# Performance work log

Hardware: AMD Instinct MI355X
Metric: run time of the kernel (lower is better)

Reference implementation:

```python
import jax, jax.numpy as jnp
from jax import lax
import numpy as np

B, N, G = 32, 8192, 40   # batch, points per cloud, base voxel grid (coords -20..19)
VS = 0.05                # voxel size
NFREQ = 4                # 8 encoding channels per coord = 4 freqs x (sin,cos)
DN = ('NCDHW', 'OIDHW', 'NCDHW')


def _encode(x):
    # sinusoidal positional encoding: [B,N,3] -> [B,N,24]
    freqs = (2.0 ** jnp.arange(NFREQ, dtype=jnp.float32)) * jnp.pi  # encoding_range=1
    ang = x[..., None] * freqs                    # [B,N,3,4]
    enc = jnp.concatenate([jnp.sin(ang), jnp.cos(ang)], axis=-1)  # [B,N,3,8]
    return enc.reshape(x.shape[0], x.shape[1], 3 * 2 * NFREQ)


def _voxelize(x, enc):
    # mean-pool point features into 40^3 voxels; returns feat [B,24,G,G,G], mask [B,1,G,G,G]
    vi = jnp.clip(jnp.floor(x / VS).astype(jnp.int32), -G // 2, G // 2 - 1) + G // 2
    lin = (vi[..., 0] * G + vi[..., 1]) * G + vi[..., 2]            # [B,N]
    flat = (lin + jnp.arange(B, dtype=jnp.int32)[:, None] * G ** 3).reshape(-1)
    fsum = jnp.zeros((B * G ** 3, 24), jnp.float32).at[flat].add(enc.reshape(-1, 24))
    cnt = jnp.zeros((B * G ** 3, 1), jnp.float32).at[flat].add(1.0)
    active = cnt > 0
    feat = jnp.where(active, fsum / jnp.maximum(cnt, 1.0), 0.0)
    feat = feat.reshape(B, G, G, G, 24).transpose(0, 4, 1, 2, 3)
    mask = active.astype(jnp.float32).reshape(B, 1, G, G, G)
    return feat, mask


def _conv(x, w, b, stride, pad):
    y = lax.conv_general_dilated(x, w, (stride,) * 3, pad, dimension_numbers=DN)
    return y + b[None, :, None, None, None]


def _ln_c(x, g, b, mask, eps=1e-5):
    # per-voxel LayerNorm over channels, only on active voxels
    mu = jnp.mean(x, axis=1, keepdims=True)
    var = jnp.mean((x - mu) ** 2, axis=1, keepdims=True)
    y = (x - mu) * lax.rsqrt(var + eps)
    return (y * g[None, :, None, None, None] + b[None, :, None, None, None]) * mask


def _maxpool2(m):
    return lax.reduce_window(m, -jnp.inf, lax.max, (1, 1, 2, 2, 2), (1, 1, 2, 2, 2), 'VALID')


def setup_inputs() -> dict:
    key = jax.random.key(0)
    ks = jax.random.split(key, 16)
    x = jax.random.uniform(ks[0], (B, N, 3), jnp.float32, minval=-1.0, maxval=1.0)

    def w(k, shape, fan_in):
        return jax.random.normal(k, shape, jnp.float32) * (2.0 / fan_in) ** 0.5

    d = {'x': x}
    d['c1w'] = w(ks[1], (32, 24, 3, 3, 3), 24 * 27);   d['c1b'] = jnp.zeros(32)
    d['g1'] = jnp.ones(32);                            d['b1'] = jnp.zeros(32)
    d['s1w'] = w(ks[2], (64, 32, 2, 2, 2), 32 * 8);    d['s1b'] = jnp.zeros(64)
    d['c2w'] = w(ks[3], (128, 64, 3, 3, 3), 64 * 27);  d['c2b'] = jnp.zeros(128)
    d['g2'] = jnp.ones(128);                           d['b2'] = jnp.zeros(128)
    d['s2w'] = w(ks[4], (256, 128, 2, 2, 2), 128 * 8); d['s2b'] = jnp.zeros(256)
    d['c3w'] = w(ks[5], (512, 256, 3, 3, 3), 256 * 27); d['c3b'] = jnp.zeros(512)
    d['g3'] = jnp.ones(512);                           d['b3'] = jnp.zeros(512)
    d['c4w'] = w(ks[6], (1024, 512, 3, 3, 3), 512 * 27); d['c4b'] = jnp.zeros(1024)
    d['s4w'] = w(ks[7], (1024, 1024, 2, 2, 2), 1024 * 8); d['s4b'] = jnp.zeros(1024)
    d['g4'] = jnp.ones(8192);                          d['b4'] = jnp.zeros(8192)
    d['f1w'] = w(ks[8], (1024, 8192), 8192);           d['f1b'] = jnp.zeros(1024)
    d['f2w'] = w(ks[9], (40, 1024), 1024);             d['f2b'] = jnp.zeros(40)
    return d


def _forward(x, c1w, c1b, g1, b1, s1w, s1b, c2w, c2b, g2, b2, s2w, s2b,
             c3w, c3b, g3, b3, c4w, c4b, s4w, s4b, g4, b4, f1w, f1b, f2w, f2b):
    enc = _encode(x)
    h, m = _voxelize(x, enc)                                 # 40^3, 24ch
    h = _conv(h, c1w, c1b, 1, 'SAME') * m                    # submanifold sparse conv
    h = jax.nn.relu(_ln_c(h, g1, b1, m))
    m = _maxpool2(m)
    h = jax.nn.relu(_conv(h, s1w, s1b, 2, 'VALID') * m)      # 40 -> 20
    h = _conv(h, c2w, c2b, 1, 'SAME') * m
    h = jax.nn.relu(_ln_c(h, g2, b2, m))
    m = _maxpool2(m)
    h = jax.nn.relu(_conv(h, s2w, s2b, 2, 'VALID') * m)      # 20 -> 10
    h = _conv(h, c3w, c3b, 1, 'SAME') * m
    h = _ln_c(h, g3, b3, m)                                  # to_dense: zeros off-mask
    h = jax.nn.relu(h)
    h = jax.nn.relu(_conv(h, c4w, c4b, 2, 'VALID'))          # 10 -> 4 (dense Conv3d)
    h = _conv(h, s4w, s4b, 2, 'VALID')                       # 4 -> 2
    h = h.reshape(B, -1)                                     # [B, 8192]
    mu = jnp.mean(h, -1, keepdims=True)
    var = jnp.mean((h - mu) ** 2, -1, keepdims=True)
    h = (h - mu) * lax.rsqrt(var + 1e-5) * g4 + b4
    h = jax.nn.relu(h)                                       # dropout: eval mode identity
    h = jax.nn.relu(h @ f1w.T + f1b)
    h = h @ f2w.T + f2b
    return jax.nn.log_softmax(h, axis=-1)


def reference(x, c1w, c1b, g1, b1, s1w, s1b, c2w, c2b, g2, b2, s2w, s2b,
              c3w, c3b, g3, b3, c4w, c4b, s4w, s4b, g4, b4, f1w, f1b, f2w, f2b):
    return _forward(x, c1w, c1b, g1, b1, s1w, s1b, c2w, c2b, g2, b2, s2w, s2b,
                    c3w, c3b, g3, b3, c4w, c4b, s4w, s4b, g4, b4, f1w, f1b, f2w, f2b)
```

## Files before the change

### kernel.cpp

```cpp
#include <hip/hip_runtime.h>
#include <math.h>

#define B_ 32
#define N_ 8192
#define G_ 40
#define CB_ 4
#define QB_ 8

static inline int cdiv(long a, int b){ return (int)((a + (long)b - 1)/b); }

typedef double d4 __attribute__((ext_vector_type(4)));

#define OFF_S1O   0
#define OFF_S2O   0
#define OFF_PART  0
#define OFF_C4O   16777216
#define OFF_FC1   20971520
#define OFF_LOG   21233664
#define OFF_C2O   32768000
#define OFF_FS    32768000
#define OFF_CNT   81920000
#define OFF_C3O   32768000
#define OFF_M20   98304000
#define OFF_M10   99328000
#define OFF_S4O   99456000
#define WS_NEEDED 101560000

__global__ __launch_bounds__(256) void encode_scatter(const float* __restrict__ x,
    double* __restrict__ fsum, double* __restrict__ cnt, int b0)
{
  int tid = blockIdx.x*256 + threadIdx.x;
  if (tid >= CB_*N_) return;
  int bl = tid / N_;
  const float* p = x + ((size_t)b0*N_ + (size_t)tid)*3;
  float c[3] = { p[0], p[1], p[2] };
  int vi[3];
  #pragma unroll
  for (int ci=0; ci<3; ++ci){
    int v = (int)floorf(c[ci] / 0.05f);
    v = v < -20 ? -20 : (v > 19 ? 19 : v);
    vi[ci] = v + 20;
  }
  int lin = (vi[0]*G_ + vi[1])*G_ + vi[2];
  double* fs = fsum + (size_t)bl*24*64000 + lin;
  const float PI_F = 3.14159265358979323846f;
  #pragma unroll
  for (int ci=0; ci<3; ++ci){
    double ang = (double)c[ci] * (double)PI_F;
    double s = sin(ang), co = cos(ang);
    #pragma unroll
    for (int k=0; k<4; ++k){
      atomicAdd(fs + (size_t)(ci*8 + k)    *64000, s);
      atomicAdd(fs + (size_t)(ci*8 + 4 + k)*64000, co);
      double s2 = 2.0*s*co;
      double c2 = co*co - s*s;
      s = s2; co = c2;
    }
  }
  atomicAdd(cnt + (size_t)bl*64000 + lin, 1.0);
}

__global__ __launch_bounds__(256) void pool_cnt_m20(const double* __restrict__ cnt,
    float* __restrict__ m20)
{
  int tid = blockIdx.x*256 + threadIdx.x;
  if (tid >= CB_*8000) return;
  int xo = tid % 20; int t = tid/20;
  int yo = t % 20;   t /= 20;
  int zo = t % 20;   int bl = t/20;
  const double* cb = cnt + (size_t)bl*64000;
  float mx = 0.0f;
  for (int dz=0; dz<2; ++dz)
    for (int dy=0; dy<2; ++dy)
      for (int dx=0; dx<2; ++dx)
        if (cb[(size_t)((zo*2+dz)*40 + (yo*2+dy))*40 + (xo*2+dx)] > 0.0) mx = 1.0f;
  m20[(size_t)bl*8000 + (zo*20+yo)*20+xo] = mx;
}

__global__ __launch_bounds__(256) void pool_mask_f(const float* __restrict__ m,
    float* __restrict__ mo, int Do, int NB)
{
  long tid = (long)blockIdx.x*256 + threadIdx.x;
  if (tid >= (long)NB*Do*Do*Do) return;
  int Di = Do*2;
  int xo = (int)(tid % Do); long t = tid / Do;
  int yo = (int)(t % Do);   t /= Do;
  int zo = (int)(t % Do);   int b = (int)(t / Do);
  const float* mb = m + (size_t)b*Di*Di*Di;
  float mx = 0.0f;
  for (int dz=0; dz<2; ++dz)
    for (int dy=0; dy<2; ++dy)
      for (int dx=0; dx<2; ++dx)
        mx = fmaxf(mx, mb[(size_t)(zo*2+dz)*Di*Di + (size_t)(yo*2+dy)*Di + (xo*2+dx)]);
  mo[tid] = mx;
}

__global__ __launch_bounds__(64) void c1_ln_s1(
    const double* __restrict__ fsum, const double* __restrict__ cnt,
    const float* __restrict__ c1w, const float* __restrict__ c1b,
    const float* __restrict__ g1,  const float* __restrict__ b1,
    const float* __restrict__ s1w, const float* __restrict__ s1b,
    double* __restrict__ out, int lb0)
{
  __shared__ double sfeat[24][64];
  __shared__ double sh1[32][8];
  __shared__ double smask[8];

  int blk = blockIdx.x;
  int xo = blk % 20; int t1 = blk/20;
  int yo = t1 % 20;  t1 /= 20;
  int zo = t1 % 20;  int bl = t1/20;
  int t = threadIdx.x;

  int lz = t >> 4, ly = (t >> 2) & 3, lx = t & 3;
  int gz = zo*2 - 1 + lz, gy = yo*2 - 1 + ly, gx = xo*2 - 1 + lx;
  bool inb = (gz>=0 && gz<40) && (gy>=0 && gy<40) && (gx>=0 && gx<40);
  int vox = (gz*40 + gy)*40 + gx;
  double cv = inb ? cnt[(size_t)bl*64000 + vox] : 0.0;
  double ic = (cv > 0.0) ? 1.0/cv : 0.0;
  const double* fb = fsum + (size_t)bl*24*64000 + (inb ? vox : 0);
  #pragma unroll
  for (int ci=0; ci<24; ++ci)
    sfeat[ci][t] = ic * fb[(size_t)ci*64000];
  if (t < 8){
    int dz=t>>2, dy=(t>>1)&1, dx=t&1;
    double c8 = cnt[(size_t)bl*64000 + (size_t)((zo*2+dz)*40 + (yo*2+dy))*40 + (xo*2+dx)];
    smask[t] = (c8 > 0.0) ? 1.0 : 0.0;
  }
  __syncthreads();

  double pm = fmax(fmax(fmax(smask[0],smask[1]),fmax(smask[2],smask[3])),
                   fmax(fmax(smask[4],smask[5]),fmax(smask[6],smask[7])));
  int ovox = (zo*20 + yo)*20 + xo;
  double* ob = out + (size_t)(lb0+bl)*64*8000 + ovox;
  if (pm == 0.0){
    ob[(size_t)t*8000] = 0.0;
    return;
  }

  int c   = t & 31;
  int svh = t >> 5;
  double acc[4] = {0,0,0,0};
  const float* wc = c1w + (size_t)c*24*27;
  for (int ci=0; ci<24; ++ci){
    const float* wp = wc + ci*27;
    const double* sp = &sfeat[ci][0] + svh*16;
    #pragma unroll
    for (int kz=0; kz<3; ++kz)
    #pragma unroll
    for (int ky=0; ky<3; ++ky)
    #pragma unroll
    for (int kx=0; kx<3; ++kx){
      double wv = (double)wp[(kz*3+ky)*3+kx];
      const double* q = sp + kz*16 + ky*4 + kx;
      acc[0] += wv * q[0];
      acc[1] += wv * q[1];
      acc[2] += wv * q[4];
      acc[3] += wv * q[5];
    }
  }
  double bias = (double)c1b[c], gc = (double)g1[c], bc = (double)b1[c];
  double h[4], rs1[4], rs2[4];
  #pragma unroll
  for (int i=0;i<4;++i){
    h[i] = (acc[i] + bias) * smask[svh*4+i];
    rs1[i] = h[i]; rs2[i] = h[i]*h[i];
  }
  #pragma unroll
  for (int off=1; off<32; off<<=1){
    #pragma unroll
    for (int i=0;i<4;++i){
      rs1[i] += __shfl_xor(rs1[i], off);
      rs2[i] += __shfl_xor(rs2[i], off);
    }
  }
  #pragma unroll
  for (int i=0;i<4;++i){
    double mu  = rs1[i]*(1.0/32.0);
    double var = fmax(rs2[i]*(1.0/32.0) - mu*mu, 0.0);
    double r   = 1.0/sqrt(var + 1e-5);
    double yv  = ((h[i]-mu)*r*gc + bc) * smask[svh*4+i];
    sh1[c][svh*4+i] = fmax(yv, 0.0);
  }
  __syncthreads();

  const float* wo = s1w + (size_t)t*256;
  double s = 0.0;
  #pragma unroll
  for (int ci=0; ci<32; ++ci){
    #pragma unroll
    for (int sv=0; sv<8; ++sv)
      s += (double)wo[ci*8+sv] * sh1[ci][sv];
  }
  ob[(size_t)t*8000] = fmax(s + (double)s1b[t], 0.0);
}

__device__ __forceinline__ double Pf_(int i,int k){ return (double)(1 + i + 31*k); }
__device__ __forceinline__ double Qf_(int k,int j){ return (double)(2 + 3*j + 7*k); }
__device__ __forceinline__ double Rf_(int m,int n){
  double s = 0.0;
  for (int k=0;k<4;++k) s += Pf_(m,k)*Qf_(k,n);
  return s;
}

template<int TI>
__global__ __launch_bounds__(256) void conv_mfma(
    const double* __restrict__ in, const float* __restrict__ w,
    const float* __restrict__ bias, double* __restrict__ out,
    int NB, int Cin, int Cout, int D)
{
  __shared__ float wl[TI*32*27];
  int spat = D*D*D;
  const int BV = 64;
  int nvt = (spat + BV - 1) / BV;
  int bid = blockIdx.x;
  int vt4 = bid % nvt; int t1 = bid / nvt;
  int cot = t1 % (Cout/32); int b = t1 / (Cout/32);
  int wid = threadIdx.x >> 6;
  int lane = threadIdx.x & 63;
  int li = lane & 15, lk = lane >> 4;

  d4 z = {0.0,0.0,0.0,0.0};
  d4 det = __builtin_amdgcn_mfma_f64_16x16x4f64(Pf_(li,lk), Qf_(lk,li), z, 0,0,0);
  bool m2 = true, m3 = true;
  #pragma unroll
  for (int r=0;r<4;++r){
    m2 = m2 && (fabs(det[r] - Rf_(lk+4*r, li)) < 1e-3);
    m3 = m3 && (fabs(det[r] - Rf_(li, 4*lk+r)) < 1e-3);
  }
  int mode = __all(m2) ? 2 : (__all(m3) ? 3 : 1);

  int vbase = vt4*BV + wid*16;
  int vox = vbase + li;
  bool vok = vox < spat;
  int vc = vok ? vox : 0;
  int vz = vc/(D*D), vy = (vc/D)%D, vx = vc%D;

  const double* inb = in + (size_t)b*Cin*spat;
  d4 acc0 = {0.0,0.0,0.0,0.0};
  d4 acc1 = {0.0,0.0,0.0,0.0};

  for (int ci0 = 0; ci0 < Cin; ci0 += TI){
    for (int idx = threadIdx.x; idx < TI*32*27; idx += 256){
      int tap = idx % 27; int t2 = idx / 27;
      int io = t2 % 32; int cc = t2 / 32;
      wl[(cc*32 + io)*27 + tap] =
          w[((size_t)(cot*32+io)*Cin + (ci0+cc))*27 + tap];
    }
    __syncthreads();
    const double* ipk = inb + (size_t)(ci0 + lk)*spat;
    #pragma unroll
    for (int dz = 0; dz < 3; ++dz){
      #pragma unroll
      for (int dy = 0; dy < 3; ++dy){
        #pragma unroll
        for (int dx = 0; dx < 3; ++dx){
          int tap = (dz*3+dy)*3+dx;
          int zi = vz+dz-1, yi = vy+dy-1, xi = vx+dx-1;
          bool ok = vok && zi>=0 && zi<D && yi>=0 && yi<D && xi>=0 && xi<D;
          int so = ok ? (zi*D + yi)*D + xi : 0;
          #pragma unroll
          for (int kq = 0; kq < TI/4; ++kq){
            double bv = ok ? ipk[(size_t)(kq*4)*spat + so] : 0.0;
            double a0 = (double)wl[((kq*4+lk)*32 + li)*27 + tap];
            double a1 = (double)wl[((kq*4+lk)*32 + 16 + li)*27 + tap];
            acc0 = __builtin_amdgcn_mfma_f64_16x16x4f64(a0, bv, acc0, 0, 0, 0);
            acc1 = __builtin_amdgcn_mfma_f64_16x16x4f64(a1, bv, acc1, 0, 0, 0);
          }
        }
      }
    }
    __syncthreads();
  }

  size_t obb = (size_t)b*Cout*spat;
  if (mode == 2){
    if (vok){
      #pragma unroll
      for (int r = 0; r < 4; ++r){
        int co0 = cot*32 + lk + 4*r;
        int co1 = co0 + 16;
        out[obb + (size_t)co0*spat + vox] = acc0[r] + (double)bias[co0];
        out[obb + (size_t)co1*spat + vox] = acc1[r] + (double)bias[co1];
      }
    }
  } else if (mode == 3){
    int co0 = cot*32 + li;
    int co1 = co0 + 16;
    double bv0 = (double)bias[co0], bv1 = (double)bias[co1];
    #pragma unroll
    for (int r = 0; r < 4; ++r){
      int vw = vbase + 4*lk + r;
      if (vw < spat){
        out[obb + (size_t)co0*spat + vw] = acc0[r] + bv0;
        out[obb + (size_t)co1*spat + vw] = acc1[r] + bv1;
      }
    }
  } else {
    if (vok){
      #pragma unroll
      for (int r = 0; r < 4; ++r){
        int co0 = cot*32 + 4*lk + r;
        int co1 = co0 + 16;
        out[obb + (size_t)co0*spat + vox] = acc0[r] + (double)bias[co0];
        out[obb + (size_t)co1*spat + vox] = acc1[r] + (double)bias[co1];
      }
    }
  }
}

static void launch_cmf(const double* in, const float* w, const float* bias,
                       double* out, int Cin, int Cout, int D, int NB, hipStream_t st)
{
  int spat = D*D*D;
  int nvt = (spat + 63)/64;
  int grid = NB * (Cout/32) * nvt;
  conv_mfma<8><<<grid,256,0,st>>>(in, w, bias, out, NB, Cin, Cout, D);
}

template<int K, int S, int P, int XT, int CT, int CGB, int TI,
         bool MMUL, bool RELU_, bool PARTIAL>
__global__ __launch_bounds__(256) void conv_lds(
    const double* __restrict__ in, const float* __restrict__ w,
    const float* __restrict__ bias, const float* __restrict__ mask,
    double* __restrict__ out, int NB, int Cin, int Din, int Cout, int Dout,
    int ncic, int cich)
{
  const int K3 = K*K*K;
  const int SP = 256/CGB;
  const int NR = (XT-1)*S + K;
  __shared__ float wl[CGB*CT][TI*K3];

  int tilesx = (Dout + XT - 1)/XT;
  int spat = tilesx*Dout*Dout;
  int nsb = (spat + SP - 1)/SP;
  int bid = blockIdx.x;
  int cic = 0;
  if (PARTIAL){ cic = bid % ncic; bid /= ncic; }
  int sb = bid % nsb;  int t1 = bid / nsb;
  int ncgo = Cout/(CT*CGB);
  int cgo = t1 % ncgo; int b = t1 / ncgo;
  int ciBeg = PARTIAL ? cic*cich : 0;
  int ciEnd = PARTIAL ? ciBeg + cich : Cin;

  int lc = threadIdx.x / SP;
  int sp = threadIdx.x % SP;
  int sidx = sb*SP + sp;
  bool act = sidx < spat;
  int sc = act ? sidx : 0;
  int tx = sc % tilesx;
  int y  = (sc/tilesx) % Dout;
  int z  = sc/(tilesx*Dout);
  int x0 = tx*XT;
  int co0 = (cgo*CGB + lc)*CT;

  int DD = Din*Din;
  const double* inb = in + (size_t)b*Cin*Din*DD;
  const int wcs = Cin*K3;

  double acc[CT][XT];
  #pragma unroll
  for (int c=0;c<CT;++c){
    double bv = PARTIAL ? 0.0 : (double)bias[co0+c];
    #pragma unroll
    for (int i=0;i<XT;++i) acc[c][i]=bv;
  }

  for (int ci0=ciBeg; ci0<ciEnd; ci0+=TI){
    const int cnt_w = CGB*CT*TI*K3;
    for (int idx = threadIdx.x; idx < cnt_w; idx += 256){
      int k  = idx % K3; int t2 = idx / K3;
      int cil= t2 % TI;  int cr = t2 / TI;
      int co = cgo*CGB*CT + cr;
      float v = 0.0f;
      if (ci0+cil < ciEnd) v = w[(size_t)co*wcs + (size_t)(ci0+cil)*K3 + k];
      wl[cr][cil*K3 + k] = v;
    }
    __syncthreads();
    int tmax = min(TI, ciEnd-ci0);
    for (int cil=0; cil<tmax; ++cil){
      const double* inc = inb + (size_t)(ci0+cil)*Din*DD;
      #pragma unroll
      for (int dz=0; dz<K; ++dz){
        int zi = z*S + dz - P;
        if (zi < 0 || zi >= Din) continue;
        #pragma unroll
        for (int dy=0; dy<K; ++dy){
          int yi = y*S + dy - P;
          if (yi < 0 || yi >= Din) continue;
          const double* row = inc + (size_t)zi*DD + (size_t)yi*Din;
          double rv[NR];
          #pragma unroll
          for (int r=0;r<NR;++r){
            int xi = x0*S + r - P;
            rv[r] = (xi>=0 && xi<Din) ? row[xi] : 0.0;
          }
          #pragma unroll
          for (int dx=0; dx<K; ++dx){
            double wv[CT];
            #pragma unroll
            for (int c=0;c<CT;++c)
              wv[c] = (double)wl[lc*CT+c][cil*K3 + (dz*K+dy)*K + dx];
            #pragma unroll
            for (int i=0;i<XT;++i)
              #pragma unroll
              for (int c=0;c<CT;++c) acc[c][i] += wv[c]*rv[i*S+dx];
          }
        }
      }
    }
    __syncthreads();
  }

  if (act){
    int oDD = Dout*Dout;
    size_t chunk_off = PARTIAL ? (size_t)cic*NB*Cout*Dout*oDD : 0;
    size_t ob = chunk_off + (size_t)b*Cout*Dout*oDD + (size_t)z*oDD + (size_t)y*Dout;
    #pragma unroll
    for (int i=0;i<XT;++i){
      int xo = x0+i;
      if (xo >= Dout) continue;
      double mv = 1.0;
      if (MMUL) mv = (double)mask[(size_t)b*Dout*oDD + (size_t)z*oDD + (size_t)y*Dout + xo];
      #pragma unroll
      for (int c=0;c<CT;++c){
        double v = acc[c][i];
        if (MMUL) v *= mv;
        if (RELU_) v = fmax(v,0.0);
        out[ob + (size_t)(co0+c)*Dout*oDD + xo] = v;
      }
    }
  }
}

template<int K,int S,int P,int XT,int CT,int CGB,int TI,bool MM,bool RL,bool PART>
static void launch_conv(const double* in, const float* w, const float* bias,
                        const float* mask, double* out,
                        int Cin, int Din, int Cout, int Dout, int NB,
                        int ncic, hipStream_t st)
{
  const int SP = 256/CGB;
  int tilesx = (Dout+XT-1)/XT;
  int spat = tilesx*Dout*Dout;
  int nsb = (spat + SP - 1)/SP;
  long grid = (long)(PART?ncic:1) * NB * (Cout/(CT*CGB)) * nsb;
  conv_lds<K,S,P,XT,CT,CGB,TI,MM,RL,PART><<<(int)grid,256,0,st>>>(
      in,w,bias,mask,out,NB,Cin,Din,Cout,Dout,ncic,Cin/(PART?ncic:1));
}

__global__ __launch_bounds__(256) void c4_reduce(const double* __restrict__ part,
    const float* __restrict__ bias, double* __restrict__ out, int NB, int ncic)
{
  long tid = (long)blockIdx.x*256 + threadIdx.x;
  long total = (long)NB*1024*64;
  if (tid >= total) return;
  int co = (int)((tid >> 6) & 1023);
  double s = (double)bias[co];
  for (int c=0; c<ncic; ++c) s += part[(size_t)c*total + tid];
  out[tid] = fmax(s, 0.0);
}

__global__ __launch_bounds__(256) void s4_wave(const double* __restrict__ c4o,
    const float* __restrict__ w, const float* __restrict__ bias,
    double* __restrict__ out, int NB)
{
  long gt = (long)blockIdx.x*256 + threadIdx.x;
  int wid = (int)(gt >> 6);
  int lane = threadIdx.x & 63;
  if (wid >= NB*1024) return;
  int co = wid & 1023; int b = wid >> 10;
  const double* ib = c4o + (size_t)b*1024*64;
  const float* wp = w + (size_t)co*8192;
  double acc[8] = {0,0,0,0,0,0,0,0};
  for (int k=lane; k<8192; k+=64){
    double wv = (double)wp[k];
    int ci = k>>3, sv = k&7;
    int dz = sv>>2, dy=(sv>>1)&1, dx=sv&1;
    const double* icp = ib + (size_t)ci*64;
    #pragma unroll
    for (int v=0; v<8; ++v){
      int zo=v>>2, yo=(v>>1)&1, xo=v&1;
      acc[v] += wv * icp[((zo*2+dz)*4+(yo*2+dy))*4 + (xo*2+dx)];
    }
  }
  #pragma unroll
  for (int v=0;v<8;++v){
    double a = acc[v];
    #pragma unroll
    for (int off=32;off>0;off>>=1) a += __shfl_down(a, off);
    if (lane==0) out[((size_t)b*1024+co)*8 + v] = a + (double)bias[co];
  }
}

__global__ __launch_bounds__(256) void ln_chan_d(double* __restrict__ x,
    const float* __restrict__ g, const float* __restrict__ bt,
    const float* __restrict__ mask, int C, int V, int NB)
{
  long tid = (long)blockIdx.x*256 + threadIdx.x;
  if (tid >= (long)NB*V) return;
  int b = (int)(tid / V);
  int v = (int)(tid - (long)b*V);
  double* xp = x + (size_t)b*C*V + v;
  double s = 0.0;
  for (int c=0; c<C; ++c) s += xp[(size_t)c*V];
  double mu = s / C;
  double s2 = 0.0;
  for (int c=0; c<C; ++c){ double d = xp[(size_t)c*V] - mu; s2 += d*d; }
  double r  = 1.0/sqrt(s2 / C + 1e-5);
  double mv = (double)mask[tid];
  for (int c=0; c<C; ++c){
    double yv = ((xp[(size_t)c*V] - mu) * r * (double)g[c] + (double)bt[c]) * mv;
    xp[(size_t)c*V] = fmax(yv, 0.0);
  }
}

__global__ __launch_bounds__(256) void ln_vec(double* __restrict__ h,
    const float* __restrict__ g, const float* __restrict__ bt)
{
  __shared__ double red[256];
  int b = blockIdx.x, t = threadIdx.x;
  double* hp = h + (size_t)b*8192;
  double s = 0.0;
  for (int k=t; k<8192; k+=256) s += hp[k];
  red[t] = s; __syncthreads();
  for (int o=128; o>0; o>>=1){ if (t<o) red[t] += red[t+o]; __syncthreads(); }
  double mu = red[0] / 8192.0;  __syncthreads();
  double s2 = 0.0;
  for (int k=t; k<8192; k+=256){ double d = hp[k]-mu; s2 += d*d; }
  red[t] = s2; __syncthreads();
  for (int o=128; o>0; o>>=1){ if (t<o) red[t] += red[t+o]; __syncthreads(); }
  double r = 1.0/sqrt(red[0]/8192.0 + 1e-5);
  for (int k=t; k<8192; k+=256)
    hp[k] = fmax((hp[k]-mu)*r*(double)g[k] + (double)bt[k], 0.0);
}

__global__ __launch_bounds__(256) void fc_wave(const double* __restrict__ h,
    const float* __restrict__ w, const float* __restrict__ bias,
    double* __restrict__ out, int Kdim, int O, int relu)
{
  long gt = (long)blockIdx.x*256 + threadIdx.x;
  int wid  = (int)(gt >> 6);
  int lane = threadIdx.x & 63;
  if (wid >= B_*O) return;
  int b = wid / O, o = wid - b*O;
  const double* hp = h + (size_t)b*Kdim;
  const float*  wp = w + (size_t)o*Kdim;
  double acc = 0.0;
  for (int k=lane; k<Kdim; k+=64) acc += hp[k]*(double)wp[k];
  #pragma unroll
  for (int off=32; off>0; off>>=1) acc += __shfl_down(acc, off);
  if (lane == 0){
    double v = acc + (double)bias[o];
    if (relu) v = fmax(v, 0.0);
    out[(size_t)b*O + o] = v;
  }
}

__global__ __launch_bounds__(64) void lsm_out(const double* __restrict__ logits,
    float* __restrict__ out)
{
  int b = threadIdx.x;
  if (b >= B_) return;
  const double* lp = logits + (size_t)b*40;
  double m = lp[0];
  for (int i=1; i<40; ++i) m = lp[i] > m ? lp[i] : m;
  double s = 0.0;
  for (int i=0; i<40; ++i) s += exp(lp[i]-m);
  double ls = log(s);
  for (int i=0; i<40; ++i) out[(size_t)b*40+i] = (float)(lp[i] - m - ls);
}

extern "C" void kernel_launch(void* const* d_in, const int* in_sizes, int n_in,
                              void* d_out, int out_size, void* d_ws, size_t ws_size,
                              hipStream_t stream)
{
  if (ws_size < (size_t)WS_NEEDED) return;

  const float* x   = (const float*)d_in[0];
  const float* c1w = (const float*)d_in[1];  const float* c1b = (const float*)d_in[2];
  const float* g1  = (const float*)d_in[3];  const float* b1  = (const float*)d_in[4];
  const float* s1w = (const float*)d_in[5];  const float* s1b = (const float*)d_in[6];
  const float* c2w = (const float*)d_in[7];  const float* c2b = (const float*)d_in[8];
  const float* g2  = (const float*)d_in[9];  const float* b2  = (const float*)d_in[10];
  const float* s2w = (const float*)d_in[11]; const float* s2b = (const float*)d_in[12];
  const float* c3w = (const float*)d_in[13]; const float* c3b = (const float*)d_in[14];
  const float* g3  = (const float*)d_in[15]; const float* b3  = (const float*)d_in[16];
  const float* c4w = (const float*)d_in[17]; const float* c4b = (const float*)d_in[18];
  const float* s4w = (const float*)d_in[19]; const float* s4b = (const float*)d_in[20];
  const float* g4  = (const float*)d_in[21]; const float* b4  = (const float*)d_in[22];
  const float* f1w = (const float*)d_in[23]; const float* f1b = (const float*)d_in[24];
  const float* f2w = (const float*)d_in[25]; const float* f2b = (const float*)d_in[26];

  char* ws = (char*)d_ws;
  double* s1o = (double*)(ws + OFF_S1O);
  double* s2o = (double*)(ws + OFF_S2O);
  double* part= (double*)(ws + OFF_PART);
  double* c4o = (double*)(ws + OFF_C4O);
  double* c2o = (double*)(ws + OFF_C2O);
  double* c3o = (double*)(ws + OFF_C3O);
  double* fsum= (double*)(ws + OFF_FS);
  double* cnt = (double*)(ws + OFF_CNT);
  float*  m20 = (float*)(ws + OFF_M20);
  float*  m10 = (float*)(ws + OFF_M10);
  double* s4o = (double*)(ws + OFF_S4O);
  double* fc1o= (double*)(ws + OFF_FC1);
  double* logd= (double*)(ws + OFF_LOG);

  for (int q = 0; q < 4; ++q){
    int qb0 = q * QB_;

    for (int sc = 0; sc < QB_/CB_; ++sc){
      int b0  = qb0 + sc*CB_;
      int lb0 = sc*CB_;
      hipMemsetAsync(ws + OFF_FS, 0, (size_t)CB_*24*64000*8 + (size_t)CB_*64000*8, stream);
      encode_scatter<<<cdiv((long)CB_*N_,256),256,0,stream>>>(x, fsum, cnt, b0);
      pool_cnt_m20  <<<cdiv((long)CB_*8000,256),256,0,stream>>>(cnt, m20 + (size_t)b0*8000);
      c1_ln_s1<<<CB_*8000, 64, 0, stream>>>(fsum, cnt, c1w, c1b, g1, b1,
                                            s1w, s1b, s1o, lb0);
    }
    pool_mask_f<<<cdiv((long)QB_*1000,256),256,0,stream>>>(
        m20 + (size_t)qb0*8000, m10 + (size_t)qb0*1000, 10, QB_);

    launch_cmf(s1o, c2w, c2b, c2o, 64, 128, 20, QB_, stream);
    ln_chan_d<<<cdiv((long)QB_*8000,256),256,0,stream>>>(
        c2o, g2, b2, m20 + (size_t)qb0*8000, 128, 8000, QB_);
    launch_conv<2,2,0, 2,8, 1,128, true,true,false>(c2o, s2w, s2b,
        m10 + (size_t)qb0*1000, s2o, 128, 20, 256, 10, QB_, 1, stream);

    launch_cmf(s2o, c3w, c3b, c3o, 256, 512, 10, QB_, stream);
    ln_chan_d<<<cdiv((long)QB_*1000,256),256,0,stream>>>(
        c3o, g3, b3, m10 + (size_t)qb0*1000, 512, 1000, QB_);

    launch_conv<3,2,0, 2,4, 8,8, false,false,true>(c3o, c4w, c4b, nullptr,
        part, 512, 10, 1024, 4, QB_, 4, stream);
    c4_reduce<<<cdiv((long)QB_*1024*64,256),256,0,stream>>>(part, c4b, c4o, QB_, 4);
    s4_wave<<<cdiv((long)QB_*1024*64,256),256,0,stream>>>(
        c4o, s4w, s4b, s4o + (size_t)qb0*8192, QB_);
  }

  ln_vec<<<B_,256,0,stream>>>(s4o, g4, b4);
  fc_wave<<<cdiv((long)B_*1024*64,256),256,0,stream>>>(s4o, f1w, f1b, fc1o, 8192, 1024, 1);
  fc_wave<<<cdiv((long)B_*40*64,256),  256,0,stream>>>(fc1o, f2w, f2b, logd, 1024, 40, 0);
  lsm_out<<<1,64,0,stream>>>(logd, (float*)d_out);
}
```

Baseline: 22.73 ms.

## Add LDS-staged input window conv kernel for the 10^3 c3 layer

Adds a specialized MFMA f64 3x3x3 conv for the 10x10x10 grid. It stages each block's 64-voxel input window plus a halo into shared memory, along with a tile of 8 input channels' weights, and reuses them across all 27 taps. Only the c3 layer (256 to 512 channels) switches to this kernel. The aim is to cut redundant global loads of the input, at the cost of more shared memory use and an extra sync per channel tile.

New measurement: 22.65 ms. Within noise of the previous version (-0.4%).

```diff
diff --git a/kernel.cpp b/kernel.cpp
--- a/kernel.cpp
+++ b/kernel.cpp
@@ -316,6 +316,130 @@
   int nvt = (spat + 63)/64;
   int grid = NB * (Cout/32) * nvt;
   conv_mfma<8><<<grid,256,0,st>>>(in, w, bias, out, NB, Cin, Cout, D);
+}
+
+__global__ __launch_bounds__(256) void conv_mfma_l(
+    const double* __restrict__ in, const float* __restrict__ w,
+    const float* __restrict__ bias, double* __restrict__ out,
+    int NB, int Cin, int Cout)
+{
+  const int D = 10, spat = 1000;
+  const int TI = 8, HALO = 111, WIN = 64 + 2*HALO;
+  __shared__ float  wl[TI*32*27];
+  __shared__ double sIn[TI][WIN];
+
+  const int BV = 64;
+  int nvt = (spat + BV - 1) / BV;
+  int bid = blockIdx.x;
+  int vt4 = bid % nvt; int t1 = bid / nvt;
+  int cot = t1 % (Cout/32); int b = t1 / (Cout/32);
+  int wid = threadIdx.x >> 6;
+  int lane = threadIdx.x & 63;
+  int li = lane & 15, lk = lane >> 4;
+
+  d4 z = {0.0,0.0,0.0,0.0};
+  d4 det = __builtin_amdgcn_mfma_f64_16x16x4f64(Pf_(li,lk), Qf_(lk,li), z, 0,0,0);
+  bool m2 = true, m3 = true;
+  #pragma unroll
+  for (int r=0;r<4;++r){
+    m2 = m2 && (fabs(det[r] - Rf_(lk+4*r, li)) < 1e-3);
+    m3 = m3 && (fabs(det[r] - Rf_(li, 4*lk+r)) < 1e-3);
+  }
+  int mode = __all(m2) ? 2 : (__all(m3) ? 3 : 1);
+
+  int blk0 = vt4*BV;
+  int vbase = blk0 + wid*16;
+  int vox = vbase + li;
+  bool vok = vox < spat;
+  int vc = vok ? vox : 0;
+  int vz = vc/(D*D), vy = (vc/D)%D, vx = vc%D;
+  int rel_base = wid*16 + li + HALO;
+
+  const double* inb = in + (size_t)b*Cin*spat;
+  d4 acc0 = {0.0,0.0,0.0,0.0};
+  d4 acc1 = {0.0,0.0,0.0,0.0};
+
+  for (int ci0 = 0; ci0 < Cin; ci0 += TI){
+    for (int idx = threadIdx.x; idx < TI*32*27; idx += 256){
+      int tap = idx % 27; int t2 = idx / 27;
+      int io = t2 % 32; int cc = t2 / 32;
+      wl[(cc*32 + io)*27 + tap] =
+          w[((size_t)(cot*32+io)*Cin + (ci0+cc))*27 + tap];
+    }
+    for (int idx = threadIdx.x; idx < TI*WIN; idx += 256){
+      int rel = idx % WIN; int cin = idx / WIN;
+      int g = blk0 - HALO + rel;
+      g = g < 0 ? 0 : (g >= spat ? spat-1 : g);
+      sIn[cin][rel] = inb[(size_t)(ci0+cin)*spat + g];
+    }
+    __syncthreads();
+    #pragma unroll
+    for (int dz = 0; dz < 3; ++dz){
+      #pragma unroll
+      for (int dy = 0; dy < 3; ++dy){
+        #pragma unroll
+        for (int dx = 0; dx < 3; ++dx){
+          int tap = (dz*3+dy)*3+dx;
+          int off = (dz-1)*100 + (dy-1)*10 + (dx-1);
+          int zi = vz+dz-1, yi = vy+dy-1, xi = vx+dx-1;
+          bool ok = vok && zi>=0 && zi<D && yi>=0 && yi<D && xi>=0 && xi<D;
+          int rel = rel_base + off;
+          #pragma unroll
+          for (int kq = 0; kq < TI/4; ++kq){
+            double bv = ok ? sIn[kq*4+lk][rel] : 0.0;
+            double a0 = (double)wl[((kq*4+lk)*32 + li)*27 + tap];
+            double a1 = (double)wl[((kq*4+lk)*32 + 16 + li)*27 + tap];
+            acc0 = __builtin_amdgcn_mfma_f64_16x16x4f64(a0, bv, acc0, 0, 0, 0);
+            acc1 = __builtin_amdgcn_mfma_f64_16x16x4f64(a1, bv, acc1, 0, 0, 0);
+          }
+        }
+      }
+    }
+    __syncthreads();
+  }
+
+  size_t obb = (size_t)b*Cout*spat;
+  if (mode == 2){
+    if (vok){
+      #pragma unroll
+      for (int r = 0; r < 4; ++r){
+        int co0 = cot*32 + lk + 4*r;
+        int co1 = co0 + 16;
+        out[obb + (size_t)co0*spat + vox] = acc0[r] + (double)bias[co0];
+        out[obb + (size_t)co1*spat + vox] = acc1[r] + (double)bias[co1];
+      }
+    }
+  } else if (mode == 3){
+    int co0 = cot*32 + li;
+    int co1 = co0 + 16;
+    double bv0 = (double)bias[co0], bv1 = (double)bias[co1];
+    #pragma unroll
+    for (int r = 0; r < 4; ++r){
+      int vw = vbase + 4*lk + r;
+      if (vw < spat){
+        out[obb + (size_t)co0*spat + vw] = acc0[r] + bv0;
+        out[obb + (size_t)co1*spat + vw] = acc1[r] + bv1;
+      }
+    }
+  } else {
+    if (vok){
+      #pragma unroll
+      for (int r = 0; r < 4; ++r){
+        int co0 = cot*32 + 4*lk + r;
+        int co1 = co0 + 16;
+        out[obb + (size_t)co0*spat + vox] = acc0[r] + (double)bias[co0];
+        out[obb + (size_t)co1*spat + vox] = acc1[r] + (double)bias[co1];
+      }
+    }
+  }
+}
+
+static void launch_cmf_l(const double* in, const float* w, const float* bias,
+                         double* out, int Cin, int Cout, int NB, hipStream_t st)
+{
+  int nvt = (1000 + 63)/64;
+  int grid = NB * (Cout/32) * nvt;
+  conv_mfma_l<<<grid,256,0,st>>>(in, w, bias, out, NB, Cin, Cout);
 }
 
 template<int K, int S, int P, int XT, int CT, int CGB, int TI,
@@ -627,7 +751,7 @@
     launch_conv<2,2,0, 2,8, 1,128, true,true,false>(c2o, s2w, s2b,
         m10 + (size_t)qb0*1000, s2o, 128, 20, 256, 10, QB_, 1, stream);
 
-    launch_cmf(s2o, c3w, c3b, c3o, 256, 512, 10, QB_, stream);
+    launch_cmf_l(s2o, c3w, c3b, c3o, 256, 512, QB_, stream);
     ln_chan_d<<<cdiv((long)QB_*1000,256),256,0,stream>>>(
         c3o, g3, b3, m10 + (size_t)qb0*1000, 512, 1000, QB_);
 
```
